# Kernel tuning notes

Hardware: AMD Instinct MI355X
Metric: run time of the kernel (lower is better)

## Reference

```python
import jax, jax.numpy as jnp
import numpy as np

B, T, D = 4096, 200, 64
NEG_INF = -(2.0 ** 32) + 1.0  # matches tf paddings constant


def setup_inputs() -> dict:
    key = jax.random.key(0)
    ks = jax.random.split(key, 12)
    queries = jax.random.normal(ks[0], (B, D), dtype=jnp.float32)
    keys = jax.random.normal(ks[1], (B, T, D), dtype=jnp.float32)
    keys_length = jax.random.randint(ks[2], (B,), 0, 200, dtype=jnp.int32)
    # attention MLP params (glorot-ish scale)
    W1 = jax.random.normal(ks[3], (4 * D, 16), dtype=jnp.float32) * (1.0 / np.sqrt(4 * D))
    b1 = jnp.zeros((16,), dtype=jnp.float32)
    W2 = jax.random.normal(ks[4], (16, 8), dtype=jnp.float32) * (1.0 / np.sqrt(16))
    b2 = jnp.zeros((8,), dtype=jnp.float32)
    W3 = jax.random.normal(ks[5], (8, 1), dtype=jnp.float32) * (1.0 / np.sqrt(8))
    b3 = jnp.zeros((1,), dtype=jnp.float32)
    W4 = jax.random.normal(ks[6], (D, D), dtype=jnp.float32) * (1.0 / np.sqrt(D))
    b4 = jnp.zeros((D,), dtype=jnp.float32)
    return {"queries": queries, "keys": keys, "keys_length": keys_length,
            "W1": W1, "b1": b1, "W2": W2, "b2": b2, "W3": W3, "b3": b3,
            "W4": W4, "b4": b4}


def reference(queries, keys, keys_length, W1, b1, W2, b2, W3, b3, W4, b4):
    Bq, Tq, Dq = keys.shape
    # tile queries across time: [B, T, D]
    q = jnp.broadcast_to(queries[:, None, :], (Bq, Tq, Dq))
    # DIN feature construction: [B, T, 4D]
    din_all = jnp.concatenate([q, keys, q - keys, q * keys], axis=-1)
    # tiny MLP scorer
    x = jax.nn.sigmoid(jnp.einsum('btf,fh->bth', din_all, W1) + b1)
    x = jax.nn.sigmoid(jnp.einsum('bth,hk->btk', x, W2) + b2)
    scores = (jnp.einsum('btk,ko->bto', x, W3) + b3)[..., 0]  # [B, T]
    # mask invalid history positions
    mask = jnp.arange(Tq, dtype=keys_length.dtype)[None, :] < keys_length[:, None]
    scores = jnp.where(mask, scores, NEG_INF)
    scores = scores / (Dq ** 0.5)  # scaling applied after masking, as in tf code
    attn = jax.nn.softmax(scores, axis=-1)  # [B, T]
    out = jnp.einsum('bt,btd->bd', attn, keys)  # weighted sum of keys
    out = out @ W4 + b4  # [B, D]
    return out
```

## Files before the change

### kernel.cpp

```cpp
#include <hip/hip_runtime.h>
#include <math.h>

#define TT 200
#define DD 64
#define MTS 72

typedef __attribute__((ext_vector_type(8))) short bf16x8;
typedef __attribute__((ext_vector_type(4))) float f32x4;

__device__ __forceinline__ float sigmoidf_(float x) {
    return 1.0f / (1.0f + __expf(-x));
}
__device__ __forceinline__ short f2bf(float x) {
    unsigned u = __float_as_uint(x);
    u += 0x7fff + ((u >> 16) & 1);
    return (short)(u >> 16);
}
__device__ __forceinline__ float bf2f(short s) {
    return __uint_as_float(((unsigned)(unsigned short)s) << 16);
}
__device__ __forceinline__ void build_hi(float4 v0, float4 v1, bf16x8& hi) {
    float xs[8] = {v0.x, v0.y, v0.z, v0.w, v1.x, v1.y, v1.z, v1.w};
    #pragma unroll
    for (int j = 0; j < 8; j++) hi[j] = f2bf(xs[j]);
}

__global__ __launch_bounds__(256) void din_attn_kernel(
    const float* __restrict__ queries,
    const float* __restrict__ keys,
    const int*   __restrict__ keys_length,
    const float* __restrict__ W1,
    const float* __restrict__ b1,
    const float* __restrict__ W2,
    const float* __restrict__ b2,
    const float* __restrict__ W3,
    const float* __restrict__ b3,
    const float* __restrict__ W4,
    const float* __restrict__ b4,
    float* __restrict__ out)
{
    __shared__ __align__(16) short MtHi[16 * MTS];
    __shared__ __align__(16) short MtLo[16 * MTS];
    __shared__ __align__(16) short H1s[208 * 16];
    __shared__ float cred[4 * 16];
    __shared__ __align__(16) float w2s[16 * 8];
    __shared__ float w3s[8];
    __shared__ float b2s[8];
    __shared__ float b3sh[1];
    __shared__ float scoresS[256];
    __shared__ float sred[8];
    __shared__ float wred[4 * 64];
    __shared__ float tmpv[64];

    const int tid  = threadIdx.x;
    const int b    = blockIdx.x;
    const int w    = tid >> 6;
    const int lane = tid & 63;
    const int m16  = lane & 15;
    const int quad = lane >> 4;
    const int len  = keys_length[b];
    const float* kb = keys + (size_t)b * (TT * DD);

    int trow0 = w * 16 + m16;
    if (trow0 > TT - 1) trow0 = TT - 1;
    const float* kp0 = kb + trow0 * 64 + quad * 8;
    float4 c0 = *(const float4*)(kp0);
    float4 c1 = *(const float4*)(kp0 + 4);
    float4 c2 = *(const float4*)(kp0 + 32);
    float4 c3 = *(const float4*)(kp0 + 36);

    {
        const int d  = tid >> 2;
        const int hg = tid & 3;
        const float q = queries[b * 64 + d];
        const float4* W1v = (const float4*)W1;
        float4 a  = W1v[(0   + d) * 4 + hg];
        float4 bb = W1v[(64  + d) * 4 + hg];
        float4 cc = W1v[(128 + d) * 4 + hg];
        float4 dd = W1v[(192 + d) * 4 + hg];
        float cp[4], mv[4];
        cp[0] = q * (a.x + cc.x);  mv[0] = bb.x - cc.x + q * dd.x;
        cp[1] = q * (a.y + cc.y);  mv[1] = bb.y - cc.y + q * dd.y;
        cp[2] = q * (a.z + cc.z);  mv[2] = bb.z - cc.z + q * dd.z;
        cp[3] = q * (a.w + cc.w);  mv[3] = bb.w - cc.w + q * dd.w;
        #pragma unroll
        for (int i = 0; i < 4; i++) {
            const int h = hg * 4 + i;
            short hi = f2bf(mv[i]);
            MtHi[h * MTS + d] = hi;
            MtLo[h * MTS + d] = f2bf(mv[i] - bf2f(hi));
        }
        #pragma unroll
        for (int mask = 4; mask <= 32; mask <<= 1) {
            #pragma unroll
            for (int i = 0; i < 4; i++) cp[i] += __shfl_xor(cp[i], mask, 64);
        }
        if (lane < 4) {
            #pragma unroll
            for (int i = 0; i < 4; i++) cred[w * 16 + lane * 4 + i] = cp[i];
        }
        if (tid < 128)       w2s[tid]        = W2[tid];
        else if (tid < 136)  w3s[tid - 128]  = W3[tid - 128];
        else if (tid < 144)  b2s[tid - 136]  = b2[tid - 136];
        else if (tid == 144) b3sh[0]         = b3[0];
    }
    __syncthreads();

    {
        const int bb0 = m16 * MTS + quad * 8;
        bf16x8 Bh0 = *(const bf16x8*)&MtHi[bb0];
        bf16x8 Bh1 = *(const bf16x8*)&MtHi[bb0 + 32];
        bf16x8 Bl0 = *(const bf16x8*)&MtLo[bb0];
        bf16x8 Bl1 = *(const bf16x8*)&MtLo[bb0 + 32];
        const float cv = b1[m16] + cred[0 + m16] + cred[16 + m16]
                       + cred[32 + m16] + cred[48 + m16];

        for (int tile = w; tile < 13; tile += 4) {
            float4 n0, n1, n2, n3;
            const int nt = tile + 4;
            if (nt < 13) {
                int trow = nt * 16 + m16;
                if (trow > TT - 1) trow = TT - 1;
                const float* kp = kb + trow * 64 + quad * 8;
                n0 = *(const float4*)(kp);
                n1 = *(const float4*)(kp + 4);
                n2 = *(const float4*)(kp + 32);
                n3 = *(const float4*)(kp + 36);
            }
            bf16x8 ah0, ah1;
            build_hi(c0, c1, ah0);
            build_hi(c2, c3, ah1);
            f32x4 acc = {0.f, 0.f, 0.f, 0.f};
            acc = __builtin_amdgcn_mfma_f32_16x16x32_bf16(ah0, Bh0, acc, 0, 0, 0);
            acc = __builtin_amdgcn_mfma_f32_16x16x32_bf16(ah0, Bl0, acc, 0, 0, 0);
            acc = __builtin_amdgcn_mfma_f32_16x16x32_bf16(ah1, Bh1, acc, 0, 0, 0);
            acc = __builtin_amdgcn_mfma_f32_16x16x32_bf16(ah1, Bl1, acc, 0, 0, 0);
            const int rb = tile * 16 + quad * 4;
            H1s[(rb + 0) * 16 + m16] = f2bf(sigmoidf_(acc[0] + cv));
            H1s[(rb + 1) * 16 + m16] = f2bf(sigmoidf_(acc[1] + cv));
            H1s[(rb + 2) * 16 + m16] = f2bf(sigmoidf_(acc[2] + cv));
            H1s[(rb + 3) * 16 + m16] = f2bf(sigmoidf_(acc[3] + cv));
            c0 = n0; c1 = n1; c2 = n2; c3 = n3;
        }
    }
    __syncthreads();

    float w4r[16];
    {
        const float* w4p = W4 + (size_t)(w * 16) * 64 + lane;
        #pragma unroll
        for (int i = 0; i < 16; i++) w4r[i] = w4p[i * 64];
    }
    float b4v = (tid < 64) ? b4[tid] : 0.0f;

    float sc = -INFINITY;
    if (tid < TT) {
        bf16x8 h1a = *(const bf16x8*)&H1s[tid * 16];
        bf16x8 h1b = *(const bf16x8*)&H1s[tid * 16 + 8];
        float hv[16];
        #pragma unroll
        for (int j = 0; j < 8; j++) { hv[j] = bf2f(h1a[j]); hv[8 + j] = bf2f(h1b[j]); }
        float s2[8];
        #pragma unroll
        for (int k = 0; k < 8; k++) s2[k] = b2s[k];
        #pragma unroll
        for (int h = 0; h < 16; h++) {
            const float hh = hv[h];
            const float4* w2r = (const float4*)&w2s[h * 8];
            float4 wa = w2r[0], wb = w2r[1];
            s2[0] = fmaf(hh, wa.x, s2[0]);
            s2[1] = fmaf(hh, wa.y, s2[1]);
            s2[2] = fmaf(hh, wa.z, s2[2]);
            s2[3] = fmaf(hh, wa.w, s2[3]);
            s2[4] = fmaf(hh, wb.x, s2[4]);
            s2[5] = fmaf(hh, wb.y, s2[5]);
            s2[6] = fmaf(hh, wb.z, s2[6]);
            s2[7] = fmaf(hh, wb.w, s2[7]);
        }
        float s3 = b3sh[0];
        #pragma unroll
        for (int k = 0; k < 8; k++) s3 = fmaf(sigmoidf_(s2[k]), w3s[k], s3);
        if (tid >= len) s3 = -4294967295.0f;
        sc = s3 * 0.125f;
    }

    float m = sc;
    #pragma unroll
    for (int off = 32; off >= 1; off >>= 1) m = fmaxf(m, __shfl_xor(m, off, 64));
    if (lane == 0) sred[w] = m;
    __syncthreads();
    m = fmaxf(fmaxf(sred[0], sred[1]), fmaxf(sred[2], sred[3]));

    float p = (tid < TT) ? __expf(sc - m) : 0.0f;
    scoresS[tid] = p;
    float ssum = p;
    #pragma unroll
    for (int off = 32; off >= 1; off >>= 1) ssum += __shfl_xor(ssum, off, 64);
    if (lane == 0) sred[4 + w] = ssum;
    __syncthreads();

    float ws = 0.0f;
    #pragma unroll 10
    for (int t = w * 50; t < w * 50 + 50; t++)
        ws = fmaf(scoresS[t], kb[t * 64 + lane], ws);
    wred[w * 64 + lane] = ws;
    __syncthreads();
    if (tid < 64) {
        const float inv = 1.0f / (sred[4] + sred[5] + sred[6] + sred[7]);
        tmpv[tid] = (wred[tid] + wred[64 + tid] + wred[128 + tid] + wred[192 + tid]) * inv;
    }
    __syncthreads();

    float po = 0.0f;
    #pragma unroll
    for (int i = 0; i < 16; i++) po = fmaf(tmpv[w * 16 + i], w4r[i], po);
    wred[w * 64 + lane] = po;
    __syncthreads();
    if (tid < 64)
        out[(size_t)b * 64 + tid] =
            b4v + wred[tid] + wred[64 + tid] + wred[128 + tid] + wred[192 + tid];
}

extern "C" void kernel_launch(void* const* d_in, const int* in_sizes, int n_in,
                              void* d_out, int out_size, void* d_ws, size_t ws_size,
                              hipStream_t stream) {
    const float* queries     = (const float*)d_in[0];
    const float* keys        = (const float*)d_in[1];
    const int*   keys_length = (const int*)  d_in[2];
    const float* W1 = (const float*)d_in[3];
    const float* b1 = (const float*)d_in[4];
    const float* W2 = (const float*)d_in[5];
    const float* b2 = (const float*)d_in[6];
    const float* W3 = (const float*)d_in[7];
    const float* b3 = (const float*)d_in[8];
    const float* W4 = (const float*)d_in[9];
    const float* b4 = (const float*)d_in[10];
    float* out = (float*)d_out;

    const int Bn = in_sizes[2];
    din_attn_kernel<<<Bn, 256, 0, stream>>>(
        queries, keys, keys_length, W1, b1, W2, b2, W3, b3, W4, b4, out);
}
```

Before: 314.9 us.

## Restructure into per-wave flash-style online softmax with length-bounded tiles

Each wavefront now handles one batch row, so a block covers four rows and the block-wide barriers give way to wave-level shuffles. The MLP scorer, online softmax and weighted sum of keys are fused into a single loop that reuses the key tile already in registers, instead of rereading keys from global memory. Only tiles up to the valid length are processed, because masked positions contribute zero weight; len==0 falls back to all tiles so the softmax stays uniform. In exchange there is more register pressure from the 16-wide output accumulators, more shuffle reductions per tile, and uneven work across waves when lengths differ.

```diff
diff --git a/kernel.cpp b/kernel.cpp
--- a/kernel.cpp
+++ b/kernel.cpp
@@ -2,7 +2,6 @@
 #include <math.h>
 
 #define TT 200
-#define DD 64
 #define MTS 72
 
 typedef __attribute__((ext_vector_type(8))) short bf16x8;
@@ -25,7 +24,7 @@
     for (int j = 0; j < 8; j++) hi[j] = f2bf(xs[j]);
 }
 
-__global__ __launch_bounds__(256) void din_attn_kernel(
+__global__ __launch_bounds__(256) void din_attn_flash(
     const float* __restrict__ queries,
     const float* __restrict__ keys,
     const int*   __restrict__ keys_length,
@@ -37,188 +36,222 @@
     const float* __restrict__ b3,
     const float* __restrict__ W4,
     const float* __restrict__ b4,
-    float* __restrict__ out)
+    float* __restrict__ out,
+    int Bn)
 {
-    __shared__ __align__(16) short MtHi[16 * MTS];
-    __shared__ __align__(16) short MtLo[16 * MTS];
-    __shared__ __align__(16) short H1s[208 * 16];
-    __shared__ float cred[4 * 16];
+    __shared__ __align__(16) short MtHi[4][16 * MTS];
+    __shared__ __align__(16) short MtLo[4][16 * MTS];
     __shared__ __align__(16) float w2s[16 * 8];
-    __shared__ float w3s[8];
-    __shared__ float b2s[8];
-    __shared__ float b3sh[1];
-    __shared__ float scoresS[256];
-    __shared__ float sred[8];
-    __shared__ float wred[4 * 64];
-    __shared__ float tmpv[64];
+    __shared__ __align__(16) float vS[4][64];
 
     const int tid  = threadIdx.x;
-    const int b    = blockIdx.x;
     const int w    = tid >> 6;
     const int lane = tid & 63;
     const int m16  = lane & 15;
     const int quad = lane >> 4;
-    const int len  = keys_length[b];
-    const float* kb = keys + (size_t)b * (TT * DD);
-
-    int trow0 = w * 16 + m16;
-    if (trow0 > TT - 1) trow0 = TT - 1;
-    const float* kp0 = kb + trow0 * 64 + quad * 8;
+
+    if (tid < 128) w2s[tid] = W2[tid];
+    __syncthreads();
+
+    const int b = blockIdx.x * 4 + w;
+    if (b >= Bn) return;
+    const int len = __builtin_amdgcn_readfirstlane(keys_length[b]);
+    const float* kb = keys + (size_t)b * (TT * 64);
+
+    float cp0 = 0.f, cp1 = 0.f, cp2 = 0.f, cp3 = 0.f;
+    {
+        const int d2 = lane >> 2;
+        const int hg = lane & 3;
+        const float4* W1v = (const float4*)W1;
+        #pragma unroll
+        for (int dg = 0; dg < 4; dg++) {
+            const int d = dg * 16 + d2;
+            const float q = queries[b * 64 + d];
+            float4 a  = W1v[(0   + d) * 4 + hg];
+            float4 bb = W1v[(64  + d) * 4 + hg];
+            float4 cc = W1v[(128 + d) * 4 + hg];
+            float4 dd = W1v[(192 + d) * 4 + hg];
+            float mv0 = bb.x - cc.x + q * dd.x;
+            float mv1 = bb.y - cc.y + q * dd.y;
+            float mv2 = bb.z - cc.z + q * dd.z;
+            float mv3 = bb.w - cc.w + q * dd.w;
+            cp0 += q * (a.x + cc.x);
+            cp1 += q * (a.y + cc.y);
+            cp2 += q * (a.z + cc.z);
+            cp3 += q * (a.w + cc.w);
+            const int hb = hg * 4;
+            short h0 = f2bf(mv0), h1 = f2bf(mv1), h2 = f2bf(mv2), h3 = f2bf(mv3);
+            MtHi[w][(hb + 0) * MTS + d] = h0;
+            MtHi[w][(hb + 1) * MTS + d] = h1;
+            MtHi[w][(hb + 2) * MTS + d] = h2;
+            MtHi[w][(hb + 3) * MTS + d] = h3;
+            MtLo[w][(hb + 0) * MTS + d] = f2bf(mv0 - bf2f(h0));
+            MtLo[w][(hb + 1) * MTS + d] = f2bf(mv1 - bf2f(h1));
+            MtLo[w][(hb + 2) * MTS + d] = f2bf(mv2 - bf2f(h2));
+            MtLo[w][(hb + 3) * MTS + d] = f2bf(mv3 - bf2f(h3));
+        }
+        #pragma unroll
+        for (int mask = 4; mask <= 32; mask <<= 1) {
+            cp0 += __shfl_xor(cp0, mask, 64);
+            cp1 += __shfl_xor(cp1, mask, 64);
+            cp2 += __shfl_xor(cp2, mask, 64);
+            cp3 += __shfl_xor(cp3, mask, 64);
+        }
+    }
+    float cv4[4];
+    cv4[0] = __shfl(cp0, quad, 64) + b1[quad * 4 + 0];
+    cv4[1] = __shfl(cp1, quad, 64) + b1[quad * 4 + 1];
+    cv4[2] = __shfl(cp2, quad, 64) + b1[quad * 4 + 2];
+    cv4[3] = __shfl(cp3, quad, 64) + b1[quad * 4 + 3];
+
+    asm volatile("" ::: "memory");
+    __builtin_amdgcn_wave_barrier();
+
+    const int bb0 = m16 * MTS + quad * 8;
+    const bf16x8 Bh0 = *(const bf16x8*)&MtHi[w][bb0];
+    const bf16x8 Bh1 = *(const bf16x8*)&MtHi[w][bb0 + 32];
+    const bf16x8 Bl0 = *(const bf16x8*)&MtLo[w][bb0];
+    const bf16x8 Bl1 = *(const bf16x8*)&MtLo[w][bb0 + 32];
+
+    const float4* w2s4 = (const float4*)w2s;
+    const float4 b2a = *(const float4*)(b2);
+    const float4 b2b = *(const float4*)(b2 + 4);
+    const float4 w3a = *(const float4*)(W3);
+    const float4 w3b = *(const float4*)(W3 + 4);
+    const float  b3v = b3[0];
+
+    float mrun = -3.0e38f;
+    float ssum = 0.0f;
+    float o[16];
+    #pragma unroll
+    for (int j = 0; j < 16; j++) o[j] = 0.0f;
+
+    const int ntiles = (len == 0) ? 13 : ((len + 15) >> 4);
+
+    const float* kp0 = kb + m16 * 64 + quad * 8;
     float4 c0 = *(const float4*)(kp0);
     float4 c1 = *(const float4*)(kp0 + 4);
     float4 c2 = *(const float4*)(kp0 + 32);
     float4 c3 = *(const float4*)(kp0 + 36);
 
-    {
-        const int d  = tid >> 2;
-        const int hg = tid & 3;
-        const float q = queries[b * 64 + d];
-        const float4* W1v = (const float4*)W1;
-        float4 a  = W1v[(0   + d) * 4 + hg];
-        float4 bb = W1v[(64  + d) * 4 + hg];
-        float4 cc = W1v[(128 + d) * 4 + hg];
-        float4 dd = W1v[(192 + d) * 4 + hg];
-        float cp[4], mv[4];
-        cp[0] = q * (a.x + cc.x);  mv[0] = bb.x - cc.x + q * dd.x;
-        cp[1] = q * (a.y + cc.y);  mv[1] = bb.y - cc.y + q * dd.y;
-        cp[2] = q * (a.z + cc.z);  mv[2] = bb.z - cc.z + q * dd.z;
-        cp[3] = q * (a.w + cc.w);  mv[3] = bb.w - cc.w + q * dd.w;
-        #pragma unroll
-        for (int i = 0; i < 4; i++) {
-            const int h = hg * 4 + i;
-            short hi = f2bf(mv[i]);
-            MtHi[h * MTS + d] = hi;
-            MtLo[h * MTS + d] = f2bf(mv[i] - bf2f(hi));
-        }
-        #pragma unroll
-        for (int mask = 4; mask <= 32; mask <<= 1) {
-            #pragma unroll
-            for (int i = 0; i < 4; i++) cp[i] += __shfl_xor(cp[i], mask, 64);
-        }
-        if (lane < 4) {
-            #pragma unroll
-            for (int i = 0; i < 4; i++) cred[w * 16 + lane * 4 + i] = cp[i];
-        }
-        if (tid < 128)       w2s[tid]        = W2[tid];
-        else if (tid < 136)  w3s[tid - 128]  = W3[tid - 128];
-        else if (tid < 144)  b2s[tid - 136]  = b2[tid - 136];
-        else if (tid == 144) b3sh[0]         = b3[0];
-    }
-    __syncthreads();
-
-    {
-        const int bb0 = m16 * MTS + quad * 8;
-        bf16x8 Bh0 = *(const bf16x8*)&MtHi[bb0];
-        bf16x8 Bh1 = *(const bf16x8*)&MtHi[bb0 + 32];
-        bf16x8 Bl0 = *(const bf16x8*)&MtLo[bb0];
-        bf16x8 Bl1 = *(const bf16x8*)&MtLo[bb0 + 32];
-        const float cv = b1[m16] + cred[0 + m16] + cred[16 + m16]
-                       + cred[32 + m16] + cred[48 + m16];
-
-        for (int tile = w; tile < 13; tile += 4) {
-            float4 n0, n1, n2, n3;
-            const int nt = tile + 4;
-            if (nt < 13) {
-                int trow = nt * 16 + m16;
-                if (trow > TT - 1) trow = TT - 1;
-                const float* kp = kb + trow * 64 + quad * 8;
-                n0 = *(const float4*)(kp);
-                n1 = *(const float4*)(kp + 4);
-                n2 = *(const float4*)(kp + 32);
-                n3 = *(const float4*)(kp + 36);
-            }
-            bf16x8 ah0, ah1;
-            build_hi(c0, c1, ah0);
-            build_hi(c2, c3, ah1);
-            f32x4 acc = {0.f, 0.f, 0.f, 0.f};
-            acc = __builtin_amdgcn_mfma_f32_16x16x32_bf16(ah0, Bh0, acc, 0, 0, 0);
-            acc = __builtin_amdgcn_mfma_f32_16x16x32_bf16(ah0, Bl0, acc, 0, 0, 0);
-            acc = __builtin_amdgcn_mfma_f32_16x16x32_bf16(ah1, Bh1, acc, 0, 0, 0);
-            acc = __builtin_amdgcn_mfma_f32_16x16x32_bf16(ah1, Bl1, acc, 0, 0, 0);
-            const int rb = tile * 16 + quad * 4;
-            H1s[(rb + 0) * 16 + m16] = f2bf(sigmoidf_(acc[0] + cv));
-            H1s[(rb + 1) * 16 + m16] = f2bf(sigmoidf_(acc[1] + cv));
-            H1s[(rb + 2) * 16 + m16] = f2bf(sigmoidf_(acc[2] + cv));
-            H1s[(rb + 3) * 16 + m16] = f2bf(sigmoidf_(acc[3] + cv));
-            c0 = n0; c1 = n1; c2 = n2; c3 = n3;
-        }
-    }
-    __syncthreads();
-
-    float w4r[16];
-    {
-        const float* w4p = W4 + (size_t)(w * 16) * 64 + lane;
-        #pragma unroll
-        for (int i = 0; i < 16; i++) w4r[i] = w4p[i * 64];
-    }
-    float b4v = (tid < 64) ? b4[tid] : 0.0f;
-
-    float sc = -INFINITY;
-    if (tid < TT) {
-        bf16x8 h1a = *(const bf16x8*)&H1s[tid * 16];
-        bf16x8 h1b = *(const bf16x8*)&H1s[tid * 16 + 8];
-        float hv[16];
-        #pragma unroll
-        for (int j = 0; j < 8; j++) { hv[j] = bf2f(h1a[j]); hv[8 + j] = bf2f(h1b[j]); }
-        float s2[8];
-        #pragma unroll
-        for (int k = 0; k < 8; k++) s2[k] = b2s[k];
-        #pragma unroll
-        for (int h = 0; h < 16; h++) {
-            const float hh = hv[h];
-            const float4* w2r = (const float4*)&w2s[h * 8];
-            float4 wa = w2r[0], wb = w2r[1];
-            s2[0] = fmaf(hh, wa.x, s2[0]);
-            s2[1] = fmaf(hh, wa.y, s2[1]);
-            s2[2] = fmaf(hh, wa.z, s2[2]);
-            s2[3] = fmaf(hh, wa.w, s2[3]);
-            s2[4] = fmaf(hh, wb.x, s2[4]);
-            s2[5] = fmaf(hh, wb.y, s2[5]);
-            s2[6] = fmaf(hh, wb.z, s2[6]);
-            s2[7] = fmaf(hh, wb.w, s2[7]);
-        }
-        float s3 = b3sh[0];
-        #pragma unroll
-        for (int k = 0; k < 8; k++) s3 = fmaf(sigmoidf_(s2[k]), w3s[k], s3);
-        if (tid >= len) s3 = -4294967295.0f;
-        sc = s3 * 0.125f;
-    }
-
-    float m = sc;
+    for (int tile = 0; tile < ntiles; tile++) {
+        float4 n0, n1, n2, n3;
+        const bool pf = (tile + 1 < ntiles);
+        if (pf) {
+            int tr = (tile + 1) * 16 + m16;
+            if (tr > TT - 1) tr = TT - 1;
+            const float* np = kb + tr * 64 + quad * 8;
+            n0 = *(const float4*)(np);
+            n1 = *(const float4*)(np + 4);
+            n2 = *(const float4*)(np + 32);
+            n3 = *(const float4*)(np + 36);
+        }
+        bf16x8 ah0, ah1;
+        build_hi(c0, c1, ah0);
+        build_hi(c2, c3, ah1);
+        f32x4 acc = {0.f, 0.f, 0.f, 0.f};
+        acc = __builtin_amdgcn_mfma_f32_16x16x32_bf16(Bh0, ah0, acc, 0, 0, 0);
+        acc = __builtin_amdgcn_mfma_f32_16x16x32_bf16(Bl0, ah0, acc, 0, 0, 0);
+        acc = __builtin_amdgcn_mfma_f32_16x16x32_bf16(Bh1, ah1, acc, 0, 0, 0);
+        acc = __builtin_amdgcn_mfma_f32_16x16x32_bf16(Bl1, ah1, acc, 0, 0, 0);
+
+        float s2[8] = {b2a.x, b2a.y, b2a.z, b2a.w, b2b.x, b2b.y, b2b.z, b2b.w};
+        #pragma unroll
+        for (int r = 0; r < 4; r++) {
+            const float h1 = sigmoidf_(acc[r] + cv4[r]);
+            const float4 wa = w2s4[(quad * 4 + r) * 2];
+            const float4 wb = w2s4[(quad * 4 + r) * 2 + 1];
+            s2[0] = fmaf(h1, wa.x, s2[0]);
+            s2[1] = fmaf(h1, wa.y, s2[1]);
+            s2[2] = fmaf(h1, wa.z, s2[2]);
+            s2[3] = fmaf(h1, wa.w, s2[3]);
+            s2[4] = fmaf(h1, wb.x, s2[4]);
+            s2[5] = fmaf(h1, wb.y, s2[5]);
+            s2[6] = fmaf(h1, wb.z, s2[6]);
+            s2[7] = fmaf(h1, wb.w, s2[7]);
+        }
+        #pragma unroll
+        for (int j = 0; j < 8; j++) {
+            s2[j] += __shfl_xor(s2[j], 16, 64);
+            s2[j] += __shfl_xor(s2[j], 32, 64);
+        }
+        float s3 = b3v;
+        s3 = fmaf(sigmoidf_(s2[0]), w3a.x, s3);
+        s3 = fmaf(sigmoidf_(s2[1]), w3a.y, s3);
+        s3 = fmaf(sigmoidf_(s2[2]), w3a.z, s3);
+        s3 = fmaf(sigmoidf_(s2[3]), w3a.w, s3);
+        s3 = fmaf(sigmoidf_(s2[4]), w3b.x, s3);
+        s3 = fmaf(sigmoidf_(s2[5]), w3b.y, s3);
+        s3 = fmaf(sigmoidf_(s2[6]), w3b.z, s3);
+        s3 = fmaf(sigmoidf_(s2[7]), w3b.w, s3);
+
+        const int tg = tile * 16 + m16;
+        float sc = s3 * 0.125f;
+        if (tg >= len) sc = -536870912.0f;
+        if (tg >= TT)  sc = -INFINITY;
+
+        float mx = sc;
+        mx = fmaxf(mx, __shfl_xor(mx, 1, 64));
+        mx = fmaxf(mx, __shfl_xor(mx, 2, 64));
+        mx = fmaxf(mx, __shfl_xor(mx, 4, 64));
+        mx = fmaxf(mx, __shfl_xor(mx, 8, 64));
+        const float mnew = fmaxf(mrun, mx);
+        const float fr = __expf(mrun - mnew);
+        const float p  = __expf(sc - mnew);
+        mrun = mnew;
+        float ps = p;
+        ps += __shfl_xor(ps, 1, 64);
+        ps += __shfl_xor(ps, 2, 64);
+        ps += __shfl_xor(ps, 4, 64);
+        ps += __shfl_xor(ps, 8, 64);
+        ssum = fmaf(ssum, fr, ps);
+        o[0]  = fmaf(o[0],  fr, p * c0.x);
+        o[1]  = fmaf(o[1],  fr, p * c0.y);
+        o[2]  = fmaf(o[2],  fr, p * c0.z);
+        o[3]  = fmaf(o[3],  fr, p * c0.w);
+        o[4]  = fmaf(o[4],  fr, p * c1.x);
+        o[5]  = fmaf(o[5],  fr, p * c1.y);
+        o[6]  = fmaf(o[6],  fr, p * c1.z);
+        o[7]  = fmaf(o[7],  fr, p * c1.w);
+        o[8]  = fmaf(o[8],  fr, p * c2.x);
+        o[9]  = fmaf(o[9],  fr, p * c2.y);
+        o[10] = fmaf(o[10], fr, p * c2.z);
+        o[11] = fmaf(o[11], fr, p * c2.w);
+        o[12] = fmaf(o[12], fr, p * c3.x);
+        o[13] = fmaf(o[13], fr, p * c3.y);
+        o[14] = fmaf(o[14], fr, p * c3.z);
+        o[15] = fmaf(o[15], fr, p * c3.w);
+
+        if (pf) { c0 = n0; c1 = n1; c2 = n2; c3 = n3; }
+    }
+
     #pragma unroll
-    for (int off = 32; off >= 1; off >>= 1) m = fmaxf(m, __shfl_xor(m, off, 64));
-    if (lane == 0) sred[w] = m;
-    __syncthreads();
-    m = fmaxf(fmaxf(sred[0], sred[1]), fmaxf(sred[2], sred[3]));
-
-    float p = (tid < TT) ? __expf(sc - m) : 0.0f;
-    scoresS[tid] = p;
-    float ssum = p;
-    #pragma unroll
-    for (int off = 32; off >= 1; off >>= 1) ssum += __shfl_xor(ssum, off, 64);
-    if (lane == 0) sred[4 + w] = ssum;
-    __syncthreads();
-
-    float ws = 0.0f;
-    #pragma unroll 10
-    for (int t = w * 50; t < w * 50 + 50; t++)
-        ws = fmaf(scoresS[t], kb[t * 64 + lane], ws);
-    wred[w * 64 + lane] = ws;
-    __syncthreads();
-    if (tid < 64) {
-        const float inv = 1.0f / (sred[4] + sred[5] + sred[6] + sred[7]);
-        tmpv[tid] = (wred[tid] + wred[64 + tid] + wred[128 + tid] + wred[192 + tid]) * inv;
-    }
-    __syncthreads();
-
-    float po = 0.0f;
-    #pragma unroll
-    for (int i = 0; i < 16; i++) po = fmaf(tmpv[w * 16 + i], w4r[i], po);
-    wred[w * 64 + lane] = po;
-    __syncthreads();
-    if (tid < 64)
-        out[(size_t)b * 64 + tid] =
-            b4v + wred[tid] + wred[64 + tid] + wred[128 + tid] + wred[192 + tid];
+    for (int mask = 1; mask <= 8; mask <<= 1) {
+        #pragma unroll
+        for (int j = 0; j < 16; j++) o[j] += __shfl_xor(o[j], mask, 64);
+    }
+    const float inv = 1.0f / ssum;
+    if (m16 == 0) {
+        #pragma unroll
+        for (int j = 0; j < 8; j++) vS[w][quad * 8 + j]      = o[j] * inv;
+        #pragma unroll
+        for (int j = 0; j < 8; j++) vS[w][32 + quad * 8 + j] = o[8 + j] * inv;
+    }
+    asm volatile("" ::: "memory");
+    __builtin_amdgcn_wave_barrier();
+
+    float po = b4[lane];
+    const float4* vS4 = (const float4*)&vS[w][0];
+    #pragma unroll 4
+    for (int d0 = 0; d0 < 16; d0++) {
+        const float4 vv = vS4[d0];
+        const float* w4p = W4 + d0 * 256 + lane;
+        po = fmaf(vv.x, w4p[0],   po);
+        po = fmaf(vv.y, w4p[64],  po);
+        po = fmaf(vv.z, w4p[128], po);
+        po = fmaf(vv.w, w4p[192], po);
+    }
+    out[(size_t)b * 64 + lane] = po;
 }
 
 extern "C" void kernel_launch(void* const* d_in, const int* in_sizes, int n_in,
@@ -238,6 +271,7 @@
     float* out = (float*)d_out;
 
     const int Bn = in_sizes[2];
-    din_attn_kernel<<<Bn, 256, 0, stream>>>(
-        queries, keys, keys_length, W1, b1, W2, b2, W3, b3, W4, b4, out);
-}
+    const int blocks = (Bn + 3) >> 2;
+    din_attn_flash<<<blocks, 256, 0, stream>>>(
+        queries, keys, keys_length, W1, b1, W2, b2, W3, b3, W4, b4, out, Bn);
+}
```

Measured after the change: 304.7 us. -3.2%, faster.
